# Performance work log

Measured on AMD Instinct MI355X. Metric: run time of the kernel, lower is better.

The kernel has to match this reference:

```python
import jax, jax.numpy as jnp
import numpy as np

K = 20
EPS = 1e-5
SLOPE = 0.2


def knn(x, k=K):
    # x: (B, C, N); returns indices of k nearest neighbors (largest -dist^2), (B, N, k)
    xx = jnp.sum(x * x, axis=1)                      # (B, N)
    inner = jnp.einsum('bcn,bcm->bnm', x, x)         # (B, N, N)
    pd = 2.0 * inner - xx[:, :, None] - xx[:, None, :]  # -squared distance
    _, idx = jax.lax.top_k(pd, k)
    return idx


def graph_feature(x, idx):
    # x: (B, C, N), idx: (B, N, k) -> (B, 2C, N): concat(x, max_k(neighbor) - x)
    feat = jnp.transpose(x, (0, 2, 1))               # (B, N, C)
    nb = jax.vmap(lambda f, i: f[i])(feat, idx)      # (B, N, k, C)
    nb_max = nb.max(axis=2)                          # (B, N, C)
    out = jnp.concatenate([feat, nb_max - feat], axis=-1)  # (B, N, 2C)
    return jnp.transpose(out, (0, 2, 1))


def conv_bn_lrelu(x, W, g, b):
    # 1x1 Conv2d (no bias) on (B,C,N,1) == channel matmul; BN2d training-mode; LeakyReLU
    h = jnp.einsum('oc,bcn->bon', W, x)              # (B, O, N)
    mu = h.mean(axis=(0, 2), keepdims=True)
    var = h.var(axis=(0, 2), keepdims=True)
    h = (h - mu) / jnp.sqrt(var + EPS) * g[None, :, None] + b[None, :, None]
    return jax.nn.leaky_relu(h, SLOPE)


def bn1d_lrelu(h, g, b):
    mu = h.mean(axis=0, keepdims=True)
    var = h.var(axis=0, keepdims=True)
    h = (h - mu) / jnp.sqrt(var + EPS) * g[None, :] + b[None, :]
    return jax.nn.leaky_relu(h, SLOPE)


def forward(x, W1, g1, b1, W2, g2, b2, W3, g3, b3, W4, g4, b4, W5, g5, b5,
            L1, g6, b6, L2, bl2, g7, b7, L3, bl3):
    B = x.shape[0]
    idx = knn(x)                                      # knn on raw xyz
    h = conv_bn_lrelu(x, W1, g1, b1)                  # (B, 64, N)
    x1 = graph_feature(h, idx)                        # (B, 128, N)

    idx = knn(x1)
    h = conv_bn_lrelu(x1, W2, g2, b2)                 # (B, 64, N)
    x2 = graph_feature(h, idx)                        # (B, 128, N)

    idx = knn(x2)
    h = conv_bn_lrelu(x2, W3, g3, b3)                 # (B, 64, N)
    x3 = graph_feature(h, idx)                        # (B, 128, N)

    idx = knn(x3)
    h = conv_bn_lrelu(x3, W4, g4, b4)                 # (B, 128, N)
    x4 = graph_feature(h, idx)                        # (B, 256, N)

    xc = jnp.concatenate([x1, x2, x3, x4], axis=1)    # (B, 640, N)
    h5 = conv_bn_lrelu(xc, W5, g5, b5)                # (B, 1024, N)
    feat = h5.max(axis=1)                             # max over CHANNELS -> (B, N=1024)

    h = bn1d_lrelu(feat @ L1.T, g6, b6)               # (B, 512); dropout=identity (eval)
    h = bn1d_lrelu(h @ L2.T + bl2, g7, b7)            # (B, 256)
    return h @ L3.T + bl3                             # (B, 40)


def setup_inputs() -> dict:
    key = jax.random.key(0)
    ks = jax.random.split(key, 32)
    ki = iter(ks)

    def rn(shape, scale=0.1):
        return jax.random.normal(next(ki), shape, dtype=jnp.float32) * scale

    def bn_params(c):
        return 1.0 + rn((c,)), rn((c,))

    x = jax.random.normal(next(ki), (32, 3, 1024), dtype=jnp.float32)
    W1 = rn((64, 3));    g1, b1 = bn_params(64)
    W2 = rn((64, 128));  g2, b2 = bn_params(64)
    W3 = rn((64, 128));  g3, b3 = bn_params(64)
    W4 = rn((128, 128)); g4, b4 = bn_params(128)
    W5 = rn((1024, 640)); g5, b5 = bn_params(1024)
    L1 = rn((512, 1024)); g6, b6 = bn_params(512)
    L2 = rn((256, 512)); bl2 = rn((256,)); g7, b7 = bn_params(256)
    L3 = rn((40, 256));  bl3 = rn((40,))
    return dict(x=x, W1=W1, g1=g1, b1=b1, W2=W2, g2=g2, b2=b2, W3=W3, g3=g3, b3=b3,
                W4=W4, g4=g4, b4=b4, W5=W5, g5=g5, b5=b5, L1=L1, g6=g6, b6=b6,
                L2=L2, bl2=bl2, g7=g7, b7=b7, L3=L3, bl3=bl3)


def reference(x, W1, g1, b1, W2, g2, b2, W3, g3, b3, W4, g4, b4, W5, g5, b5,
              L1, g6, b6, L2, bl2, g7, b7, L3, bl3):
    return forward(x, W1, g1, b1, W2, g2, b2, W3, g3, b3, W4, g4, b4, W5, g5, b5,
                   L1, g6, b6, L2, bl2, g7, b7, L3, bl3)
```

## Files before the change

### kernel.cpp

```cpp
#include <hip/hip_runtime.h>
#include <cfloat>
#include <cstdint>

#define NB 32
#define NPTS 1024
#define KNN 20
#define RTOT (NB * NPTS)

typedef __attribute__((ext_vector_type(8))) short bf16x8;
typedef __attribute__((ext_vector_type(4))) float f32x4;

__device__ __forceinline__ float lrelu(float v) { return v >= 0.f ? v : 0.2f * v; }

__global__ void k_transpose_x(const float* __restrict__ x, float* __restrict__ xT) {
    int g = blockIdx.x * 256 + threadIdx.x;
    if (g >= NB * 3 * NPTS) return;
    int n = g % NPTS;
    int c = (g / NPTS) % 3;
    int b = g / (3 * NPTS);
    xT[((size_t)b * NPTS + n) * 3 + c] = x[g];
}

__global__ void k_xx(const float* __restrict__ X, int ldx, int C, float* __restrict__ xx) {
    int r = blockIdx.x * 256 + threadIdx.x;
    if (r >= RTOT) return;
    const float* p = X + (size_t)r * ldx;
    float s = 0.f;
    for (int c = 0; c < C; ++c) { float v = p[c]; s += v * v; }
    xx[r] = s;
}

__global__ __launch_bounds__(256) void k_gemm_xwt(
    const float* __restrict__ X, int ldx, int K,
    const float* __restrict__ W,
    float* __restrict__ H, int ldh)
{
    __shared__ float As[16][68];
    __shared__ float Bs[16][68];
    int tid = threadIdx.x;
    int tx = tid & 15, ty = tid >> 4;
    int c0 = blockIdx.x * 64;
    int r0 = blockIdx.y * 64;
    float acc[4][4] = {};
    int lr = tid >> 4, lk = tid & 15;
    for (int k0 = 0; k0 < K; k0 += 16) {
#pragma unroll
        for (int i = 0; i < 4; ++i) {
            int row = lr + i * 16;
            int kk = k0 + lk;
            float av = 0.f, bv = 0.f;
            if (kk < K) {
                av = X[(size_t)(r0 + row) * ldx + kk];
                bv = W[(size_t)(c0 + row) * K + kk];
            }
            As[lk][row] = av;
            Bs[lk][row] = bv;
        }
        __syncthreads();
#pragma unroll
        for (int k = 0; k < 16; ++k) {
            float4 a4 = *(const float4*)&As[k][ty * 4];
            float4 b4 = *(const float4*)&Bs[k][tx * 4];
            float av[4] = {a4.x, a4.y, a4.z, a4.w};
            float bv[4] = {b4.x, b4.y, b4.z, b4.w};
#pragma unroll
            for (int i = 0; i < 4; ++i)
#pragma unroll
                for (int j = 0; j < 4; ++j)
                    acc[i][j] = fmaf(av[i], bv[j], acc[i][j]);
        }
        __syncthreads();
    }
#pragma unroll
    for (int i = 0; i < 4; ++i) {
        float4 v = make_float4(acc[i][0], acc[i][1], acc[i][2], acc[i][3]);
        *(float4*)&H[(size_t)(r0 + ty * 4 + i) * ldh + c0 + tx * 4] = v;
    }
}

template<int K>
__global__ __launch_bounds__(256) void k_pd_sym(
    const float* __restrict__ X, int ldx,
    const float* __restrict__ xx, float* __restrict__ pd)
{
    __shared__ float As[16][132];
    __shared__ float Bs[16][132];
    int b = blockIdx.y;
    int tid = threadIdx.x;
    int tx = tid & 15, ty = tid >> 4;
    int t = blockIdx.x, rb = 0, rem = 8;
    while (t >= rem) { t -= rem; ++rb; --rem; }
    int cb = rb + t;
    int r0 = rb * 128, c0 = cb * 128;
    const float* Xb = X + (size_t)b * NPTS * ldx;
    int lk = tid & 15, lr = tid >> 4;
    float acc[8][8] = {};
    for (int k0 = 0; k0 < K; k0 += 16) {
#pragma unroll
        for (int i = 0; i < 8; ++i) {
            int row = lr + i * 16;
            int kk = k0 + lk;
            float av = 0.f, bv = 0.f;
            if (kk < K) {
                av = Xb[(size_t)(r0 + row) * ldx + kk];
                bv = Xb[(size_t)(c0 + row) * ldx + kk];
            }
            As[lk][row] = av;
            Bs[lk][row] = bv;
        }
        __syncthreads();
#pragma unroll
        for (int k = 0; k < 16; ++k) {
            float a[8], bb[8];
            *(float4*)&a[0]  = *(const float4*)&As[k][ty * 4];
            *(float4*)&a[4]  = *(const float4*)&As[k][64 + ty * 4];
            *(float4*)&bb[0] = *(const float4*)&Bs[k][tx * 4];
            *(float4*)&bb[4] = *(const float4*)&Bs[k][64 + tx * 4];
#pragma unroll
            for (int i = 0; i < 8; ++i)
#pragma unroll
                for (int j = 0; j < 8; ++j)
                    acc[i][j] = fmaf(a[i], bb[j], acc[i][j]);
        }
        __syncthreads();
    }
    const float* xxb = xx + (size_t)b * NPTS;
    float* pdb = pd + (size_t)b * NPTS * NPTS;
    float xc[8];
#pragma unroll
    for (int j = 0; j < 8; ++j)
        xc[j] = xxb[c0 + ((j < 4) ? (tx * 4 + j) : (64 + tx * 4 + j - 4))];
    float xr[8];
#pragma unroll
    for (int i = 0; i < 8; ++i)
        xr[i] = xxb[r0 + ((i < 4) ? (ty * 4 + i) : (64 + ty * 4 + i - 4))];
#pragma unroll
    for (int i = 0; i < 8; ++i) {
        int r = r0 + ((i < 4) ? (ty * 4 + i) : (64 + ty * 4 + i - 4));
        float* orow = &pdb[(size_t)r * NPTS + c0];
        float4 v0, v1;
        v0.x = 2.f * acc[i][0] - xr[i] - xc[0];
        v0.y = 2.f * acc[i][1] - xr[i] - xc[1];
        v0.z = 2.f * acc[i][2] - xr[i] - xc[2];
        v0.w = 2.f * acc[i][3] - xr[i] - xc[3];
        v1.x = 2.f * acc[i][4] - xr[i] - xc[4];
        v1.y = 2.f * acc[i][5] - xr[i] - xc[5];
        v1.z = 2.f * acc[i][6] - xr[i] - xc[6];
        v1.w = 2.f * acc[i][7] - xr[i] - xc[7];
        *(float4*)&orow[tx * 4]      = v0;
        *(float4*)&orow[64 + tx * 4] = v1;
    }
    if (cb > rb) {
#pragma unroll
        for (int j = 0; j < 8; ++j) {
            int c = c0 + ((j < 4) ? (tx * 4 + j) : (64 + tx * 4 + j - 4));
            float* orow = &pdb[(size_t)c * NPTS + r0];
            float4 w0, w1;
            w0.x = 2.f * acc[0][j] - xc[j] - xr[0];
            w0.y = 2.f * acc[1][j] - xc[j] - xr[1];
            w0.z = 2.f * acc[2][j] - xc[j] - xr[2];
            w0.w = 2.f * acc[3][j] - xc[j] - xr[3];
            w1.x = 2.f * acc[4][j] - xc[j] - xr[4];
            w1.y = 2.f * acc[5][j] - xc[j] - xr[5];
            w1.z = 2.f * acc[6][j] - xc[j] - xr[6];
            w1.w = 2.f * acc[7][j] - xc[j] - xr[7];
            *(float4*)&orow[ty * 4]      = w0;
            *(float4*)&orow[64 + ty * 4] = w1;
        }
    }
}

__global__ __launch_bounds__(256) void k_topk_wave(const float* __restrict__ pd, int* __restrict__ idx) {
    int wid = (blockIdx.x * 256 + threadIdx.x) >> 6;
    int lane = threadIdx.x & 63;
    const float* row = pd + (size_t)wid * NPTS;
    float v[16];
#pragma unroll
    for (int j = 0; j < 16; ++j) v[j] = row[lane + 64 * j];
    float bv = v[0]; int bj = 0;
#pragma unroll
    for (int j = 1; j < 16; ++j) if (v[j] > bv) { bv = v[j]; bj = j; }
    int* out = idx + (size_t)wid * KNN;
    for (int kk = 0; kk < KNN; ++kk) {
        float cv = bv;
        int ci = lane + (bj << 6);
#pragma unroll
        for (int s = 1; s < 64; s <<= 1) {
            float ov = __shfl_xor(cv, s);
            int oi = __shfl_xor(ci, s);
            if (ov > cv || (ov == cv && oi < ci)) { cv = ov; ci = oi; }
        }
        if (lane == 0) out[kk] = ci;
        bool mine = (ci & 63) == lane;
        int jdead = ci >> 6;
#pragma unroll
        for (int j = 0; j < 16; ++j) if (mine && j == jdead) v[j] = -FLT_MAX;
        bv = v[0]; bj = 0;
#pragma unroll
        for (int j = 1; j < 16; ++j) if (v[j] > bv) { bv = v[j]; bj = j; }
    }
}

__device__ __forceinline__ void split2(float x, ushort& h, ushort& l) {
    uint u = __float_as_uint(x);
    uint r = u + 0x7FFFu + ((u >> 16) & 1u);
    ushort hh = (ushort)(r >> 16);
    float hf = __uint_as_float((uint)hh << 16);
    float d = x - hf;
    uint u2 = __float_as_uint(d);
    uint r2 = u2 + 0x7FFFu + ((u2 >> 16) & 1u);
    h = hh;
    l = (ushort)(r2 >> 16);
}

__device__ __forceinline__ uint pack2(ushort a, ushort b) { return (uint)a | ((uint)b << 16); }

__device__ __forceinline__ void stage_split(const float* __restrict__ g,
                                            ushort* __restrict__ dh, ushort* __restrict__ dl) {
    float4 v0 = *(const float4*)(g);
    float4 v1 = *(const float4*)(g + 4);
    float4 v2 = *(const float4*)(g + 8);
    float4 v3 = *(const float4*)(g + 12);
    float xs[16] = {v0.x, v0.y, v0.z, v0.w, v1.x, v1.y, v1.z, v1.w,
                    v2.x, v2.y, v2.z, v2.w, v3.x, v3.y, v3.z, v3.w};
    ushort h[16], l[16];
#pragma unroll
    for (int i = 0; i < 16; ++i) split2(xs[i], h[i], l[i]);
    uint4 H0, H1, L0, L1;
    H0.x = pack2(h[0], h[1]);  H0.y = pack2(h[2], h[3]);
    H0.z = pack2(h[4], h[5]);  H0.w = pack2(h[6], h[7]);
    H1.x = pack2(h[8], h[9]);  H1.y = pack2(h[10], h[11]);
    H1.z = pack2(h[12], h[13]); H1.w = pack2(h[14], h[15]);
    L0.x = pack2(l[0], l[1]);  L0.y = pack2(l[2], l[3]);
    L0.z = pack2(l[4], l[5]);  L0.w = pack2(l[6], l[7]);
    L1.x = pack2(l[8], l[9]);  L1.y = pack2(l[10], l[11]);
    L1.z = pack2(l[12], l[13]); L1.w = pack2(l[14], l[15]);
    *(uint4*)(dh)     = H0;
    *(uint4*)(dh + 8) = H1;
    *(uint4*)(dl)     = L0;
    *(uint4*)(dl + 8) = L1;
}

__global__ void k_split(const float* __restrict__ X, ushort* __restrict__ Xh,
                        ushort* __restrict__ Xl, int n) {
    int g = (blockIdx.x * 256 + threadIdx.x) * 8;
    if (g >= n) return;
    float4 a = *(const float4*)(X + g);
    float4 b = *(const float4*)(X + g + 4);
    float xs[8] = {a.x, a.y, a.z, a.w, b.x, b.y, b.z, b.w};
    ushort h[8], l[8];
#pragma unroll
    for (int i = 0; i < 8; ++i) split2(xs[i], h[i], l[i]);
    uint4 H, L;
    H.x = pack2(h[0], h[1]); H.y = pack2(h[2], h[3]);
    H.z = pack2(h[4], h[5]); H.w = pack2(h[6], h[7]);
    L.x = pack2(l[0], l[1]); L.y = pack2(l[2], l[3]);
    L.z = pack2(l[4], l[5]); L.w = pack2(l[6], l[7]);
    *(uint4*)(Xh + g) = H;
    *(uint4*)(Xl + g) = L;
}

#define LDK 40
__global__ __launch_bounds__(256) void k_gemm5_mfma(
    const float* __restrict__ X, const ushort* __restrict__ Wh, const ushort* __restrict__ Wl,
    float* __restrict__ H, float* __restrict__ sums)
{
    __shared__ __align__(16) ushort sAh[128 * LDK];
    __shared__ __align__(16) ushort sAl[128 * LDK];
    __shared__ __align__(16) ushort sBh[128 * LDK];
    __shared__ __align__(16) ushort sBl[128 * LDK];
    int tid = threadIdx.x;
    int lane = tid & 63, w = tid >> 6;
    int wm = w >> 1, wn = w & 1;
    int bid = blockIdx.x;
    int wg = (bid & 7) * 256 + (bid >> 3);
    int cb = wg & 7, rb = wg >> 3;
    int r0 = rb * 128, c0 = cb * 128;
    int srow = tid >> 1, sk = (tid & 1) * 16;
    int fr = lane & 15;
    int kg = (lane >> 4) << 3;
    f32x4 acc[4][4] = {};
    for (int k0 = 0; k0 < 640; k0 += 32) {
        stage_split(X + (size_t)(r0 + srow) * 640 + k0 + sk,
                    &sAh[srow * LDK + sk], &sAl[srow * LDK + sk]);
        {
            size_t gb = (size_t)(c0 + srow) * 640 + k0 + sk;
            *(uint4*)&sBh[srow * LDK + sk]     = *(const uint4*)(Wh + gb);
            *(uint4*)&sBh[srow * LDK + sk + 8] = *(const uint4*)(Wh + gb + 8);
            *(uint4*)&sBl[srow * LDK + sk]     = *(const uint4*)(Wl + gb);
            *(uint4*)&sBl[srow * LDK + sk + 8] = *(const uint4*)(Wl + gb + 8);
        }
        __syncthreads();
        bf16x8 ah[4], al[4];
#pragma unroll
        for (int mi = 0; mi < 4; ++mi) {
            int rr = wm * 64 + mi * 16 + fr;
            ah[mi] = *(const bf16x8*)&sAh[rr * LDK + kg];
            al[mi] = *(const bf16x8*)&sAl[rr * LDK + kg];
        }
#pragma unroll
        for (int ni = 0; ni < 4; ++ni) {
            int cc = wn * 64 + ni * 16 + fr;
            bf16x8 bh = *(const bf16x8*)&sBh[cc * LDK + kg];
            bf16x8 bl = *(const bf16x8*)&sBl[cc * LDK + kg];
#pragma unroll
            for (int mi = 0; mi < 4; ++mi) {
                acc[mi][ni] = __builtin_amdgcn_mfma_f32_16x16x32_bf16(ah[mi], bh, acc[mi][ni], 0, 0, 0);
                acc[mi][ni] = __builtin_amdgcn_mfma_f32_16x16x32_bf16(ah[mi], bl, acc[mi][ni], 0, 0, 0);
                acc[mi][ni] = __builtin_amdgcn_mfma_f32_16x16x32_bf16(al[mi], bh, acc[mi][ni], 0, 0, 0);
            }
        }
        __syncthreads();
    }
#pragma unroll
    for (int mi = 0; mi < 4; ++mi) {
        int rg = r0 + wm * 64 + mi * 16 + (lane >> 4) * 4;
#pragma unroll
        for (int ni = 0; ni < 4; ++ni) {
            int cg = c0 + wn * 64 + ni * 16 + fr;
#pragma unroll
            for (int r = 0; r < 4; ++r)
                H[(size_t)(rg + r) * 1024 + cg] = acc[mi][ni][r];
        }
    }
    float* csum  = (float*)sAh;
    float* csum2 = csum + 128;
    if (tid < 128) { csum[tid] = 0.f; csum2[tid] = 0.f; }
    __syncthreads();
#pragma unroll
    for (int ni = 0; ni < 4; ++ni) {
        float s = 0.f, s2 = 0.f;
#pragma unroll
        for (int mi = 0; mi < 4; ++mi)
#pragma unroll
            for (int r = 0; r < 4; ++r) { float v = acc[mi][ni][r]; s += v; s2 += v * v; }
        int c = wn * 64 + ni * 16 + fr;
        atomicAdd(&csum[c], s);
        atomicAdd(&csum2[c], s2);
    }
    __syncthreads();
    if (tid < 128) {
        atomicAdd(&sums[c0 + tid], csum[tid]);
        atomicAdd(&sums[1024 + c0 + tid], csum2[tid]);
    }
}

__global__ __launch_bounds__(256) void k_bn_stats(const float* __restrict__ H, int ldh, int O, int R,
                                                  float* __restrict__ sums) {
    int nblk = gridDim.x;
    int rows = (R + nblk - 1) / nblk;
    int r0 = blockIdx.x * rows;
    int r1 = r0 + rows; if (r1 > R) r1 = R;
    int tid = threadIdx.x;
    if (O <= 256) {
        int per = 256 / O;
        int c = tid % O;
        int rOff = tid / O;
        float s = 0.f, s2 = 0.f;
        for (int r = r0 + rOff; r < r1; r += per) {
            float v = H[(size_t)r * ldh + c];
            s += v; s2 += v * v;
        }
        __shared__ float ls[256], ls2[256];
        ls[tid] = s; ls2[tid] = s2;
        __syncthreads();
        for (int st = 128; st >= O; st >>= 1) {
            if (tid < st) { ls[tid] += ls[tid + st]; ls2[tid] += ls2[tid + st]; }
            __syncthreads();
        }
        if (tid < O) {
            atomicAdd(&sums[c], ls[tid]);
            atomicAdd(&sums[O + c], ls2[tid]);
        }
    } else {
        int nc = O / 256;
        float s[4] = {0, 0, 0, 0}, s2[4] = {0, 0, 0, 0};
        for (int r = r0; r < r1; ++r) {
            const float* rowp = H + (size_t)r * ldh;
            for (int i = 0; i < nc; ++i) {
                float v = rowp[tid + i * 256];
                s[i] += v; s2[i] += v * v;
            }
        }
        for (int i = 0; i < nc; ++i) {
            atomicAdd(&sums[tid + i * 256], s[i]);
            atomicAdd(&sums[O + tid + i * 256], s2[i]);
        }
    }
}

__global__ void k_bn_finalize(const float* __restrict__ sums, const float* __restrict__ g,
                              const float* __restrict__ bta, int O, float invR,
                              float* __restrict__ ss) {
    int o = blockIdx.x * 256 + threadIdx.x;
    if (o >= O) return;
    float mu = sums[o] * invR;
    float var = sums[O + o] * invR - mu * mu;
    float sc = g[o] / sqrtf(var + 1e-5f);
    ss[o] = sc;
    ss[O + o] = bta[o] - mu * sc;
}

__global__ __launch_bounds__(256) void k_graph_feature(
    const float* __restrict__ hT, int ldh, int C,
    const int* __restrict__ idx, const float* __restrict__ ss,
    float* __restrict__ out, int ldo, int colOff)
{
    int ppb = 256 / C;
    int p = threadIdx.x / C;
    int c = threadIdx.x % C;
    int r = blockIdx.x * ppb + p;
    int b = r >> 10;
    float sc = ss[c], sh = ss[C + c];
    float self = hT[(size_t)r * ldh + c];
    float vs = lrelu(sc * self + sh);
    const int* ip = idx + (size_t)r * KNN;
    float m = -FLT_MAX;
#pragma unroll 4
    for (int k = 0; k < KNN; ++k) {
        int j = ip[k];
        float hv = hT[((size_t)b * NPTS + j) * ldh + c];
        float v = lrelu(sc * hv + sh);
        m = fmaxf(m, v);
    }
    float* orow = out + (size_t)r * ldo + colOff;
    orow[c] = vs;
    orow[C + c] = m - vs;
}

__global__ __launch_bounds__(256) void k_chanmax(const float* __restrict__ h5,
                                                 const float* __restrict__ ss,
                                                 float* __restrict__ feat) {
    int r = blockIdx.x;
    int tid = threadIdx.x;
    __shared__ float red[256];
    const float* rowp = h5 + (size_t)r * 1024;
    float m = -FLT_MAX;
    for (int o = tid; o < 1024; o += 256) {
        float v = lrelu(ss[o] * rowp[o] + ss[1024 + o]);
        m = fmaxf(m, v);
    }
    red[tid] = m;
    __syncthreads();
    for (int s = 128; s > 0; s >>= 1) {
        if (tid < s) red[tid] = fmaxf(red[tid], red[tid + s]);
        __syncthreads();
    }
    if (tid == 0) feat[r] = red[0];
}

__global__ void k_fc(const float* __restrict__ in, const float* __restrict__ Lw,
                     const float* __restrict__ bias, float* __restrict__ out, int K, int J) {
    int g = blockIdx.x * 256 + threadIdx.x;
    if (g >= 32 * J) return;
    int b = g / J, j = g % J;
    const float* xr = in + (size_t)b * K;
    const float* wr = Lw + (size_t)j * K;
    float acc = 0.f;
    for (int k = 0; k < K; ++k) acc = fmaf(xr[k], wr[k], acc);
    out[g] = bias ? acc + bias[j] : acc;
}

__global__ void k_bn1d(float* __restrict__ h, const float* __restrict__ g,
                       const float* __restrict__ bta, int J) {
    int j = blockIdx.x * 256 + threadIdx.x;
    if (j >= J) return;
    float s = 0.f, s2 = 0.f;
    for (int b = 0; b < 32; ++b) {
        float v = h[b * J + j];
        s += v; s2 += v * v;
    }
    float mu = s / 32.f;
    float var = s2 / 32.f - mu * mu;
    float sc = g[j] / sqrtf(var + 1e-5f);
    float sh = bta[j] - mu * sc;
    for (int b = 0; b < 32; ++b) {
        float v = sc * h[b * J + j] + sh;
        h[b * J + j] = lrelu(v);
    }
}

extern "C" void kernel_launch(void* const* d_in, const int* in_sizes, int n_in,
                              void* d_out, int out_size, void* d_ws, size_t ws_size,
                              hipStream_t stream) {
    const float* x   = (const float*)d_in[0];
    const float* W1  = (const float*)d_in[1];
    const float* g1  = (const float*)d_in[2];
    const float* b1  = (const float*)d_in[3];
    const float* W2  = (const float*)d_in[4];
    const float* g2  = (const float*)d_in[5];
    const float* b2  = (const float*)d_in[6];
    const float* W3  = (const float*)d_in[7];
    const float* g3  = (const float*)d_in[8];
    const float* b3  = (const float*)d_in[9];
    const float* W4  = (const float*)d_in[10];
    const float* g4  = (const float*)d_in[11];
    const float* b4  = (const float*)d_in[12];
    const float* W5  = (const float*)d_in[13];
    const float* g5  = (const float*)d_in[14];
    const float* b5  = (const float*)d_in[15];
    const float* L1  = (const float*)d_in[16];
    const float* g6  = (const float*)d_in[17];
    const float* b6  = (const float*)d_in[18];
    const float* L2  = (const float*)d_in[19];
    const float* bl2 = (const float*)d_in[20];
    const float* g7  = (const float*)d_in[21];
    const float* b7  = (const float*)d_in[22];
    const float* L3  = (const float*)d_in[23];
    const float* bl3 = (const float*)d_in[24];

    float* ws = (float*)d_ws;
    size_t off = 0;
    auto alloc = [&](size_t n) { size_t o = off; off += (n + 63) & ~(size_t)63; return o; };
    float* pd   = ws + alloc((size_t)NB * NPTS * NPTS);
    float* h5   = pd;
    float* xcT  = ws + alloc((size_t)RTOT * 640);
    float* hbuf = ws + alloc((size_t)RTOT * 128);
    float* xT   = ws + alloc((size_t)RTOT * 3);
    float* xxb  = ws + alloc(RTOT);
    float* sums = ws + alloc(2048);
    float* ss   = ws + alloc(2048);
    float* feat = ws + alloc(RTOT);
    float* h1   = ws + alloc(32 * 512);
    float* h2   = ws + alloc(32 * 256);
    int*   idxb = (int*)(ws + alloc((size_t)RTOT * KNN));
    ushort* W5h = (ushort*)(ws + alloc(1024 * 640 / 2));
    ushort* W5l = (ushort*)(ws + alloc(1024 * 640 / 2));

    k_transpose_x<<<(NB * 3 * NPTS + 255) / 256, 256, 0, stream>>>(x, xT);
    k_split<<<(1024 * 640 / 8 + 255) / 256, 256, 0, stream>>>(W5, W5h, W5l, 1024 * 640);

    auto run_knn = [&](const float* X, int ldx, int C) {
        k_xx<<<(RTOT + 255) / 256, 256, 0, stream>>>(X, ldx, C, xxb);
        if (C == 3)
            k_pd_sym<3><<<dim3(36, NB), 256, 0, stream>>>(X, ldx, xxb, pd);
        else
            k_pd_sym<128><<<dim3(36, NB), 256, 0, stream>>>(X, ldx, xxb, pd);
        k_topk_wave<<<RTOT / 4, 256, 0, stream>>>(pd, idxb);
    };
    auto run_conv = [&](const float* X, int ldx, int K, const float* W,
                        const float* g, const float* bta, int O) {
        k_gemm_xwt<<<dim3(O / 64, RTOT / 64), 256, 0, stream>>>(X, ldx, K, W, hbuf, O);
        hipMemsetAsync(sums, 0, 2 * O * sizeof(float), stream);
        k_bn_stats<<<256, 256, 0, stream>>>(hbuf, O, O, RTOT, sums);
        k_bn_finalize<<<(O + 255) / 256, 256, 0, stream>>>(sums, g, bta, O, 1.f / RTOT, ss);
    };
    auto run_gf = [&](int C, int colOff) {
        int ppb = 256 / C;
        k_graph_feature<<<RTOT / ppb, 256, 0, stream>>>(hbuf, C, C, idxb, ss, xcT, 640, colOff);
    };

    run_knn(xT, 3, 3);
    run_conv(xT, 3, 3, W1, g1, b1, 64);
    run_gf(64, 0);

    run_knn(xcT + 0, 640, 128);
    run_conv(xcT + 0, 640, 128, W2, g2, b2, 64);
    run_gf(64, 128);

    run_knn(xcT + 128, 640, 128);
    run_conv(xcT + 128, 640, 128, W3, g3, b3, 64);
    run_gf(64, 256);

    run_knn(xcT + 256, 640, 128);
    run_conv(xcT + 256, 640, 128, W4, g4, b4, 128);
    run_gf(128, 384);

    hipMemsetAsync(sums, 0, 2048 * sizeof(float), stream);
    k_gemm5_mfma<<<2048, 256, 0, stream>>>(xcT, W5h, W5l, h5, sums);
    k_bn_finalize<<<4, 256, 0, stream>>>(sums, g5, b5, 1024, 1.f / RTOT, ss);
    k_chanmax<<<RTOT, 256, 0, stream>>>(h5, ss, feat);

    k_fc<<<(32 * 512 + 255) / 256, 256, 0, stream>>>(feat, L1, nullptr, h1, 1024, 512);
    k_bn1d<<<(512 + 255) / 256, 256, 0, stream>>>(h1, g6, b6, 512);
    k_fc<<<(32 * 256 + 255) / 256, 256, 0, stream>>>(h1, L2, bl2, h2, 512, 256);
    k_bn1d<<<(256 + 255) / 256, 256, 0, stream>>>(h2, g7, b7, 256);
    k_fc<<<(32 * 40 + 255) / 256, 256, 0, stream>>>(h2, L3, bl3, (float*)d_out, 256, 40);
}
```

Measured before the change: 1.678 ms.

## Pre-split xcT into bf16 hi/lo in graph_feature and consolidate BN memsets

The graph feature kernel now also writes bf16 hi/lo splits of its outputs, so the final 640->1024 GEMM can load pre-split operands instead of splitting fp32 activations in every tile iteration (each A tile is re-split by all 8 column blocks). The per-conv memsets of the BN sum buffers are replaced by one upfront memset over separate per-layer sum slots. This adds extra global writes in graph_feature and depends on the workspace being large enough, with a fallback to the old GEMM otherwise.

```diff
diff --git a/kernel.cpp b/kernel.cpp
--- a/kernel.cpp
+++ b/kernel.cpp
@@ -261,6 +261,69 @@
 }
 
 #define LDK 40
+
+__device__ __forceinline__ void gemm5_core(
+    int tid, const ushort* sAh, const ushort* sAl, const ushort* sBh, const ushort* sBl,
+    f32x4 (&acc)[4][4], int wm, int wn, int fr, int kg)
+{
+    bf16x8 ah[4], al[4];
+#pragma unroll
+    for (int mi = 0; mi < 4; ++mi) {
+        int rr = wm * 64 + mi * 16 + fr;
+        ah[mi] = *(const bf16x8*)&sAh[rr * LDK + kg];
+        al[mi] = *(const bf16x8*)&sAl[rr * LDK + kg];
+    }
+#pragma unroll
+    for (int ni = 0; ni < 4; ++ni) {
+        int cc = wn * 64 + ni * 16 + fr;
+        bf16x8 bh = *(const bf16x8*)&sBh[cc * LDK + kg];
+        bf16x8 bl = *(const bf16x8*)&sBl[cc * LDK + kg];
+#pragma unroll
+        for (int mi = 0; mi < 4; ++mi) {
+            acc[mi][ni] = __builtin_amdgcn_mfma_f32_16x16x32_bf16(ah[mi], bh, acc[mi][ni], 0, 0, 0);
+            acc[mi][ni] = __builtin_amdgcn_mfma_f32_16x16x32_bf16(ah[mi], bl, acc[mi][ni], 0, 0, 0);
+            acc[mi][ni] = __builtin_amdgcn_mfma_f32_16x16x32_bf16(al[mi], bh, acc[mi][ni], 0, 0, 0);
+        }
+    }
+}
+
+__device__ __forceinline__ void gemm5_epilogue(
+    int tid, int lane, int wm, int wn, int fr, int r0, int c0,
+    f32x4 (&acc)[4][4], float* H, float* sums, ushort* scratch)
+{
+#pragma unroll
+    for (int mi = 0; mi < 4; ++mi) {
+        int rg = r0 + wm * 64 + mi * 16 + (lane >> 4) * 4;
+#pragma unroll
+        for (int ni = 0; ni < 4; ++ni) {
+            int cg = c0 + wn * 64 + ni * 16 + fr;
+#pragma unroll
+            for (int r = 0; r < 4; ++r)
+                H[(size_t)(rg + r) * 1024 + cg] = acc[mi][ni][r];
+        }
+    }
+    float* csum  = (float*)scratch;
+    float* csum2 = csum + 128;
+    if (tid < 128) { csum[tid] = 0.f; csum2[tid] = 0.f; }
+    __syncthreads();
+#pragma unroll
+    for (int ni = 0; ni < 4; ++ni) {
+        float s = 0.f, s2 = 0.f;
+#pragma unroll
+        for (int mi = 0; mi < 4; ++mi)
+#pragma unroll
+            for (int r = 0; r < 4; ++r) { float v = acc[mi][ni][r]; s += v; s2 += v * v; }
+        int c = wn * 64 + ni * 16 + fr;
+        atomicAdd(&csum[c], s);
+        atomicAdd(&csum2[c], s2);
+    }
+    __syncthreads();
+    if (tid < 128) {
+        atomicAdd(&sums[c0 + tid], csum[tid]);
+        atomicAdd(&sums[1024 + c0 + tid], csum2[tid]);
+    }
+}
+
 __global__ __launch_bounds__(256) void k_gemm5_mfma(
     const float* __restrict__ X, const ushort* __restrict__ Wh, const ushort* __restrict__ Wl,
     float* __restrict__ H, float* __restrict__ sums)
@@ -291,58 +354,48 @@
             *(uint4*)&sBl[srow * LDK + sk + 8] = *(const uint4*)(Wl + gb + 8);
         }
         __syncthreads();
-        bf16x8 ah[4], al[4];
-#pragma unroll
-        for (int mi = 0; mi < 4; ++mi) {
-            int rr = wm * 64 + mi * 16 + fr;
-            ah[mi] = *(const bf16x8*)&sAh[rr * LDK + kg];
-            al[mi] = *(const bf16x8*)&sAl[rr * LDK + kg];
-        }
-#pragma unroll
-        for (int ni = 0; ni < 4; ++ni) {
-            int cc = wn * 64 + ni * 16 + fr;
-            bf16x8 bh = *(const bf16x8*)&sBh[cc * LDK + kg];
-            bf16x8 bl = *(const bf16x8*)&sBl[cc * LDK + kg];
-#pragma unroll
-            for (int mi = 0; mi < 4; ++mi) {
-                acc[mi][ni] = __builtin_amdgcn_mfma_f32_16x16x32_bf16(ah[mi], bh, acc[mi][ni], 0, 0, 0);
-                acc[mi][ni] = __builtin_amdgcn_mfma_f32_16x16x32_bf16(ah[mi], bl, acc[mi][ni], 0, 0, 0);
-                acc[mi][ni] = __builtin_amdgcn_mfma_f32_16x16x32_bf16(al[mi], bh, acc[mi][ni], 0, 0, 0);
-            }
-        }
-        __syncthreads();
-    }
-#pragma unroll
-    for (int mi = 0; mi < 4; ++mi) {
-        int rg = r0 + wm * 64 + mi * 16 + (lane >> 4) * 4;
-#pragma unroll
-        for (int ni = 0; ni < 4; ++ni) {
-            int cg = c0 + wn * 64 + ni * 16 + fr;
-#pragma unroll
-            for (int r = 0; r < 4; ++r)
-                H[(size_t)(rg + r) * 1024 + cg] = acc[mi][ni][r];
-        }
-    }
-    float* csum  = (float*)sAh;
-    float* csum2 = csum + 128;
-    if (tid < 128) { csum[tid] = 0.f; csum2[tid] = 0.f; }
-    __syncthreads();
-#pragma unroll
-    for (int ni = 0; ni < 4; ++ni) {
-        float s = 0.f, s2 = 0.f;
-#pragma unroll
-        for (int mi = 0; mi < 4; ++mi)
-#pragma unroll
-            for (int r = 0; r < 4; ++r) { float v = acc[mi][ni][r]; s += v; s2 += v * v; }
-        int c = wn * 64 + ni * 16 + fr;
-        atomicAdd(&csum[c], s);
-        atomicAdd(&csum2[c], s2);
-    }
-    __syncthreads();
-    if (tid < 128) {
-        atomicAdd(&sums[c0 + tid], csum[tid]);
-        atomicAdd(&sums[1024 + c0 + tid], csum2[tid]);
-    }
+        gemm5_core(tid, sAh, sAl, sBh, sBl, acc, wm, wn, fr, kg);
+        __syncthreads();
+    }
+    gemm5_epilogue(tid, lane, wm, wn, fr, r0, c0, acc, H, sums, sAh);
+}
+
+__global__ __launch_bounds__(256) void k_gemm5_pre(
+    const ushort* __restrict__ Ah, const ushort* __restrict__ Al,
+    const ushort* __restrict__ Wh, const ushort* __restrict__ Wl,
+    float* __restrict__ H, float* __restrict__ sums)
+{
+    __shared__ __align__(16) ushort sAh[128 * LDK];
+    __shared__ __align__(16) ushort sAl[128 * LDK];
+    __shared__ __align__(16) ushort sBh[128 * LDK];
+    __shared__ __align__(16) ushort sBl[128 * LDK];
+    int tid = threadIdx.x;
+    int lane = tid & 63, w = tid >> 6;
+    int wm = w >> 1, wn = w & 1;
+    int bid = blockIdx.x;
+    int wg = (bid & 7) * 256 + (bid >> 3);
+    int cb = wg & 7, rb = wg >> 3;
+    int r0 = rb * 128, c0 = cb * 128;
+    int srow = tid >> 1, sk = (tid & 1) * 16;
+    int fr = lane & 15;
+    int kg = (lane >> 4) << 3;
+    f32x4 acc[4][4] = {};
+    for (int k0 = 0; k0 < 640; k0 += 32) {
+        size_t ga = (size_t)(r0 + srow) * 640 + k0 + sk;
+        *(uint4*)&sAh[srow * LDK + sk]     = *(const uint4*)(Ah + ga);
+        *(uint4*)&sAh[srow * LDK + sk + 8] = *(const uint4*)(Ah + ga + 8);
+        *(uint4*)&sAl[srow * LDK + sk]     = *(const uint4*)(Al + ga);
+        *(uint4*)&sAl[srow * LDK + sk + 8] = *(const uint4*)(Al + ga + 8);
+        size_t gb = (size_t)(c0 + srow) * 640 + k0 + sk;
+        *(uint4*)&sBh[srow * LDK + sk]     = *(const uint4*)(Wh + gb);
+        *(uint4*)&sBh[srow * LDK + sk + 8] = *(const uint4*)(Wh + gb + 8);
+        *(uint4*)&sBl[srow * LDK + sk]     = *(const uint4*)(Wl + gb);
+        *(uint4*)&sBl[srow * LDK + sk + 8] = *(const uint4*)(Wl + gb + 8);
+        __syncthreads();
+        gemm5_core(tid, sAh, sAl, sBh, sBl, acc, wm, wn, fr, kg);
+        __syncthreads();
+    }
+    gemm5_epilogue(tid, lane, wm, wn, fr, r0, c0, acc, H, sums, sAh);
 }
 
 __global__ __launch_bounds__(256) void k_bn_stats(const float* __restrict__ H, int ldh, int O, int R,
@@ -404,7 +457,8 @@
 __global__ __launch_bounds__(256) void k_graph_feature(
     const float* __restrict__ hT, int ldh, int C,
     const int* __restrict__ idx, const float* __restrict__ ss,
-    float* __restrict__ out, int ldo, int colOff)
+    float* __restrict__ out, int ldo, int colOff,
+    ushort* __restrict__ outh, ushort* __restrict__ outl)
 {
     int ppb = 256 / C;
     int p = threadIdx.x / C;
@@ -423,9 +477,17 @@
         float v = lrelu(sc * hv + sh);
         m = fmaxf(m, v);
     }
-    float* orow = out + (size_t)r * ldo + colOff;
-    orow[c] = vs;
-    orow[C + c] = m - vs;
+    float diff = m - vs;
+    size_t base = (size_t)r * ldo + colOff;
+    out[base + c] = vs;
+    out[base + C + c] = diff;
+    if (outh) {
+        ushort hh, ll;
+        split2(vs, hh, ll);
+        outh[base + c] = hh; outl[base + c] = ll;
+        split2(diff, hh, ll);
+        outh[base + C + c] = hh; outl[base + C + c] = ll;
+    }
 }
 
 __global__ __launch_bounds__(256) void k_chanmax(const float* __restrict__ h5,
@@ -518,7 +580,7 @@
     float* hbuf = ws + alloc((size_t)RTOT * 128);
     float* xT   = ws + alloc((size_t)RTOT * 3);
     float* xxb  = ws + alloc(RTOT);
-    float* sums = ws + alloc(2048);
+    float* sumsA = ws + alloc(2048 * 5);
     float* ss   = ws + alloc(2048);
     float* feat = ws + alloc(RTOT);
     float* h1   = ws + alloc(32 * 512);
@@ -526,9 +588,18 @@
     int*   idxb = (int*)(ws + alloc((size_t)RTOT * KNN));
     ushort* W5h = (ushort*)(ws + alloc(1024 * 640 / 2));
     ushort* W5l = (ushort*)(ws + alloc(1024 * 640 / 2));
+    size_t base_floats = off;
+    size_t presplit_floats = base_floats + 2 * ((size_t)RTOT * 320 + 64);
+    bool use_pre = (presplit_floats * sizeof(float) <= ws_size);
+    ushort* xcTh = nullptr; ushort* xcTl = nullptr;
+    if (use_pre) {
+        xcTh = (ushort*)(ws + alloc((size_t)RTOT * 320));
+        xcTl = (ushort*)(ws + alloc((size_t)RTOT * 320));
+    }
 
     k_transpose_x<<<(NB * 3 * NPTS + 255) / 256, 256, 0, stream>>>(x, xT);
     k_split<<<(1024 * 640 / 8 + 255) / 256, 256, 0, stream>>>(W5, W5h, W5l, 1024 * 640);
+    hipMemsetAsync(sumsA, 0, 2048 * 5 * sizeof(float), stream);
 
     auto run_knn = [&](const float* X, int ldx, int C) {
         k_xx<<<(RTOT + 255) / 256, 256, 0, stream>>>(X, ldx, C, xxb);
@@ -539,36 +610,39 @@
         k_topk_wave<<<RTOT / 4, 256, 0, stream>>>(pd, idxb);
     };
     auto run_conv = [&](const float* X, int ldx, int K, const float* W,
-                        const float* g, const float* bta, int O) {
+                        const float* g, const float* bta, int O, float* sums) {
         k_gemm_xwt<<<dim3(O / 64, RTOT / 64), 256, 0, stream>>>(X, ldx, K, W, hbuf, O);
-        hipMemsetAsync(sums, 0, 2 * O * sizeof(float), stream);
         k_bn_stats<<<256, 256, 0, stream>>>(hbuf, O, O, RTOT, sums);
         k_bn_finalize<<<(O + 255) / 256, 256, 0, stream>>>(sums, g, bta, O, 1.f / RTOT, ss);
     };
     auto run_gf = [&](int C, int colOff) {
         int ppb = 256 / C;
-        k_graph_feature<<<RTOT / ppb, 256, 0, stream>>>(hbuf, C, C, idxb, ss, xcT, 640, colOff);
+        k_graph_feature<<<RTOT / ppb, 256, 0, stream>>>(hbuf, C, C, idxb, ss, xcT, 640, colOff,
+                                                        xcTh, xcTl);
     };
 
     run_knn(xT, 3, 3);
-    run_conv(xT, 3, 3, W1, g1, b1, 64);
+    run_conv(xT, 3, 3, W1, g1, b1, 64, sumsA);
     run_gf(64, 0);
 
     run_knn(xcT + 0, 640, 128);
-    run_conv(xcT + 0, 640, 128, W2, g2, b2, 64);
+    run_conv(xcT + 0, 640, 128, W2, g2, b2, 64, sumsA + 2048);
     run_gf(64, 128);
 
     run_knn(xcT + 128, 640, 128);
-    run_conv(xcT + 128, 640, 128, W3, g3, b3, 64);
+    run_conv(xcT + 128, 640, 128, W3, g3, b3, 64, sumsA + 4096);
     run_gf(64, 256);
 
     run_knn(xcT + 256, 640, 128);
-    run_conv(xcT + 256, 640, 128, W4, g4, b4, 128);
+    run_conv(xcT + 256, 640, 128, W4, g4, b4, 128, sumsA + 6144);
     run_gf(128, 384);
 
-    hipMemsetAsync(sums, 0, 2048 * sizeof(float), stream);
-    k_gemm5_mfma<<<2048, 256, 0, stream>>>(xcT, W5h, W5l, h5, sums);
-    k_bn_finalize<<<4, 256, 0, stream>>>(sums, g5, b5, 1024, 1.f / RTOT, ss);
+    float* sums5 = sumsA + 8192;
+    if (use_pre)
+        k_gemm5_pre<<<2048, 256, 0, stream>>>(xcTh, xcTl, W5h, W5l, h5, sums5);
+    else
+        k_gemm5_mfma<<<2048, 256, 0, stream>>>(xcT, W5h, W5l, h5, sums5);
+    k_bn_finalize<<<4, 256, 0, stream>>>(sums5, g5, b5, 1024, 1.f / RTOT, ss);
     k_chanmax<<<RTOT, 256, 0, stream>>>(h5, ss, feat);
 
     k_fc<<<(32 * 512 + 255) / 256, 256, 0, stream>>>(feat, L1, nullptr, h1, 1024, 512);
```

Measured after the change: 1.759 ms. 4.9% more time.

## Widen gemm5 tile to 128x256 with 512 threads and batch BN-sum memsets

Applied to the files above, without the earlier changes.

The W5 MFMA GEMM now uses 512-thread blocks, each computing a 128x256 output tile with 8 waves in a 2x4 layout. This halves the block count and the number of times each A tile is split and staged, improving reuse of the fp32-to-bf16 split A data. Separately, the five per-layer BN-sum memsets are replaced by one memset of a combined buffer at the start, which removes four small launches. In exchange the larger tile raises LDS and register pressure per block, which may lower occupancy.

```diff
diff --git a/kernel.cpp b/kernel.cpp
--- a/kernel.cpp
+++ b/kernel.cpp
@@ -215,38 +215,10 @@
 
 __device__ __forceinline__ uint pack2(ushort a, ushort b) { return (uint)a | ((uint)b << 16); }
 
-__device__ __forceinline__ void stage_split(const float* __restrict__ g,
-                                            ushort* __restrict__ dh, ushort* __restrict__ dl) {
-    float4 v0 = *(const float4*)(g);
-    float4 v1 = *(const float4*)(g + 4);
-    float4 v2 = *(const float4*)(g + 8);
-    float4 v3 = *(const float4*)(g + 12);
-    float xs[16] = {v0.x, v0.y, v0.z, v0.w, v1.x, v1.y, v1.z, v1.w,
-                    v2.x, v2.y, v2.z, v2.w, v3.x, v3.y, v3.z, v3.w};
-    ushort h[16], l[16];
-#pragma unroll
-    for (int i = 0; i < 16; ++i) split2(xs[i], h[i], l[i]);
-    uint4 H0, H1, L0, L1;
-    H0.x = pack2(h[0], h[1]);  H0.y = pack2(h[2], h[3]);
-    H0.z = pack2(h[4], h[5]);  H0.w = pack2(h[6], h[7]);
-    H1.x = pack2(h[8], h[9]);  H1.y = pack2(h[10], h[11]);
-    H1.z = pack2(h[12], h[13]); H1.w = pack2(h[14], h[15]);
-    L0.x = pack2(l[0], l[1]);  L0.y = pack2(l[2], l[3]);
-    L0.z = pack2(l[4], l[5]);  L0.w = pack2(l[6], l[7]);
-    L1.x = pack2(l[8], l[9]);  L1.y = pack2(l[10], l[11]);
-    L1.z = pack2(l[12], l[13]); L1.w = pack2(l[14], l[15]);
-    *(uint4*)(dh)     = H0;
-    *(uint4*)(dh + 8) = H1;
-    *(uint4*)(dl)     = L0;
-    *(uint4*)(dl + 8) = L1;
-}
-
-__global__ void k_split(const float* __restrict__ X, ushort* __restrict__ Xh,
-                        ushort* __restrict__ Xl, int n) {
-    int g = (blockIdx.x * 256 + threadIdx.x) * 8;
-    if (g >= n) return;
-    float4 a = *(const float4*)(X + g);
-    float4 b = *(const float4*)(X + g + 4);
+__device__ __forceinline__ void stage_split8(const float* __restrict__ g,
+                                             ushort* __restrict__ dh, ushort* __restrict__ dl) {
+    float4 a = *(const float4*)(g);
+    float4 b = *(const float4*)(g + 4);
     float xs[8] = {a.x, a.y, a.z, a.w, b.x, b.y, b.z, b.w};
     ushort h[8], l[8];
 #pragma unroll
@@ -256,39 +228,47 @@
     H.z = pack2(h[4], h[5]); H.w = pack2(h[6], h[7]);
     L.x = pack2(l[0], l[1]); L.y = pack2(l[2], l[3]);
     L.z = pack2(l[4], l[5]); L.w = pack2(l[6], l[7]);
-    *(uint4*)(Xh + g) = H;
-    *(uint4*)(Xl + g) = L;
+    *(uint4*)(dh) = H;
+    *(uint4*)(dl) = L;
+}
+
+__global__ void k_split(const float* __restrict__ X, ushort* __restrict__ Xh,
+                        ushort* __restrict__ Xl, int n) {
+    int g = (blockIdx.x * 256 + threadIdx.x) * 8;
+    if (g >= n) return;
+    stage_split8(X + g, Xh + g, Xl + g);
 }
 
 #define LDK 40
-__global__ __launch_bounds__(256) void k_gemm5_mfma(
+__global__ __launch_bounds__(512) void k_gemm5_mfma(
     const float* __restrict__ X, const ushort* __restrict__ Wh, const ushort* __restrict__ Wl,
     float* __restrict__ H, float* __restrict__ sums)
 {
     __shared__ __align__(16) ushort sAh[128 * LDK];
     __shared__ __align__(16) ushort sAl[128 * LDK];
-    __shared__ __align__(16) ushort sBh[128 * LDK];
-    __shared__ __align__(16) ushort sBl[128 * LDK];
+    __shared__ __align__(16) ushort sBh[256 * LDK];
+    __shared__ __align__(16) ushort sBl[256 * LDK];
     int tid = threadIdx.x;
     int lane = tid & 63, w = tid >> 6;
-    int wm = w >> 1, wn = w & 1;
+    int wm = w >> 2, wn = w & 3;
     int bid = blockIdx.x;
-    int wg = (bid & 7) * 256 + (bid >> 3);
-    int cb = wg & 7, rb = wg >> 3;
-    int r0 = rb * 128, c0 = cb * 128;
-    int srow = tid >> 1, sk = (tid & 1) * 16;
+    int wg = (bid & 7) * 128 + (bid >> 3);
+    int cb = wg & 3, rb = wg >> 2;
+    int r0 = rb * 128, c0 = cb * 256;
+    int srA = tid >> 2, skA = (tid & 3) * 8;
+    int srB = tid >> 1, skB = (tid & 1) * 16;
     int fr = lane & 15;
     int kg = (lane >> 4) << 3;
     f32x4 acc[4][4] = {};
     for (int k0 = 0; k0 < 640; k0 += 32) {
-        stage_split(X + (size_t)(r0 + srow) * 640 + k0 + sk,
-                    &sAh[srow * LDK + sk], &sAl[srow * LDK + sk]);
+        stage_split8(X + (size_t)(r0 + srA) * 640 + k0 + skA,
+                     &sAh[srA * LDK + skA], &sAl[srA * LDK + skA]);
         {
-            size_t gb = (size_t)(c0 + srow) * 640 + k0 + sk;
-            *(uint4*)&sBh[srow * LDK + sk]     = *(const uint4*)(Wh + gb);
-            *(uint4*)&sBh[srow * LDK + sk + 8] = *(const uint4*)(Wh + gb + 8);
-            *(uint4*)&sBl[srow * LDK + sk]     = *(const uint4*)(Wl + gb);
-            *(uint4*)&sBl[srow * LDK + sk + 8] = *(const uint4*)(Wl + gb + 8);
+            size_t gb = (size_t)(c0 + srB) * 640 + k0 + skB;
+            *(uint4*)&sBh[srB * LDK + skB]     = *(const uint4*)(Wh + gb);
+            *(uint4*)&sBh[srB * LDK + skB + 8] = *(const uint4*)(Wh + gb + 8);
+            *(uint4*)&sBl[srB * LDK + skB]     = *(const uint4*)(Wl + gb);
+            *(uint4*)&sBl[srB * LDK + skB + 8] = *(const uint4*)(Wl + gb + 8);
         }
         __syncthreads();
         bf16x8 ah[4], al[4];
@@ -324,8 +304,8 @@
         }
     }
     float* csum  = (float*)sAh;
-    float* csum2 = csum + 128;
-    if (tid < 128) { csum[tid] = 0.f; csum2[tid] = 0.f; }
+    float* csum2 = csum + 256;
+    if (tid < 256) { csum[tid] = 0.f; csum2[tid] = 0.f; }
     __syncthreads();
 #pragma unroll
     for (int ni = 0; ni < 4; ++ni) {
@@ -339,7 +319,7 @@
         atomicAdd(&csum2[c], s2);
     }
     __syncthreads();
-    if (tid < 128) {
+    if (tid < 256) {
         atomicAdd(&sums[c0 + tid], csum[tid]);
         atomicAdd(&sums[1024 + c0 + tid], csum2[tid]);
     }
@@ -518,7 +498,7 @@
     float* hbuf = ws + alloc((size_t)RTOT * 128);
     float* xT   = ws + alloc((size_t)RTOT * 3);
     float* xxb  = ws + alloc(RTOT);
-    float* sums = ws + alloc(2048);
+    float* sumsA = ws + alloc(2048 * 5);
     float* ss   = ws + alloc(2048);
     float* feat = ws + alloc(RTOT);
     float* h1   = ws + alloc(32 * 512);
@@ -529,6 +509,7 @@
 
     k_transpose_x<<<(NB * 3 * NPTS + 255) / 256, 256, 0, stream>>>(x, xT);
     k_split<<<(1024 * 640 / 8 + 255) / 256, 256, 0, stream>>>(W5, W5h, W5l, 1024 * 640);
+    hipMemsetAsync(sumsA, 0, 2048 * 5 * sizeof(float), stream);
 
     auto run_knn = [&](const float* X, int ldx, int C) {
         k_xx<<<(RTOT + 255) / 256, 256, 0, stream>>>(X, ldx, C, xxb);
@@ -539,9 +520,8 @@
         k_topk_wave<<<RTOT / 4, 256, 0, stream>>>(pd, idxb);
     };
     auto run_conv = [&](const float* X, int ldx, int K, const float* W,
-                        const float* g, const float* bta, int O) {
+                        const float* g, const float* bta, int O, float* sums) {
         k_gemm_xwt<<<dim3(O / 64, RTOT / 64), 256, 0, stream>>>(X, ldx, K, W, hbuf, O);
-        hipMemsetAsync(sums, 0, 2 * O * sizeof(float), stream);
         k_bn_stats<<<256, 256, 0, stream>>>(hbuf, O, O, RTOT, sums);
         k_bn_finalize<<<(O + 255) / 256, 256, 0, stream>>>(sums, g, bta, O, 1.f / RTOT, ss);
     };
@@ -551,24 +531,24 @@
     };
 
     run_knn(xT, 3, 3);
-    run_conv(xT, 3, 3, W1, g1, b1, 64);
+    run_conv(xT, 3, 3, W1, g1, b1, 64, sumsA);
     run_gf(64, 0);
 
     run_knn(xcT + 0, 640, 128);
-    run_conv(xcT + 0, 640, 128, W2, g2, b2, 64);
+    run_conv(xcT + 0, 640, 128, W2, g2, b2, 64, sumsA + 2048);
     run_gf(64, 128);
 
     run_knn(xcT + 128, 640, 128);
-    run_conv(xcT + 128, 640, 128, W3, g3, b3, 64);
+    run_conv(xcT + 128, 640, 128, W3, g3, b3, 64, sumsA + 4096);
     run_gf(64, 256);
 
     run_knn(xcT + 256, 640, 128);
-    run_conv(xcT + 256, 640, 128, W4, g4, b4, 128);
+    run_conv(xcT + 256, 640, 128, W4, g4, b4, 128, sumsA + 6144);
     run_gf(128, 384);
 
-    hipMemsetAsync(sums, 0, 2048 * sizeof(float), stream);
-    k_gemm5_mfma<<<2048, 256, 0, stream>>>(xcT, W5h, W5l, h5, sums);
-    k_bn_finalize<<<4, 256, 0, stream>>>(sums, g5, b5, 1024, 1.f / RTOT, ss);
+    float* sums5 = sumsA + 8192;
+    k_gemm5_mfma<<<1024, 512, 0, stream>>>(xcT, W5h, W5l, h5, sums5);
+    k_bn_finalize<<<4, 256, 0, stream>>>(sums5, g5, b5, 1024, 1.f / RTOT, ss);
     k_chanmax<<<RTOT, 256, 0, stream>>>(h5, ss, feat);
 
     k_fc<<<(32 * 512 + 255) / 256, 256, 0, stream>>>(feat, L1, nullptr, h1, 1024, 512);
```

Result: no change. 1.661 ms (-1.0%).
